# Performance work log

Hardware: AMD Instinct MI355X
Metric: run time of the kernel (lower is better)

Reference implementation:

```python
import jax, jax.numpy as jnp
import numpy as np

DIM = 1024
NUM_HEADS = 16
HEAD_DIM = DIM // NUM_HEADS

def setup_inputs() -> dict:
    key = jax.random.key(0)
    ks = jax.random.split(key, 5)
    s = 1.0 / np.sqrt(DIM)
    x = jax.random.normal(ks[0], (2, 2048, DIM), dtype=jnp.float32)
    W_qkv = jax.random.uniform(ks[1], (DIM, 3 * DIM), dtype=jnp.float32, minval=-s, maxval=s)
    b_qkv = jax.random.uniform(ks[2], (3 * DIM,), dtype=jnp.float32, minval=-s, maxval=s)
    W_out = jax.random.uniform(ks[3], (DIM, DIM), dtype=jnp.float32, minval=-s, maxval=s)
    b_out = jax.random.uniform(ks[4], (DIM,), dtype=jnp.float32, minval=-s, maxval=s)
    return {"x": x, "W_qkv": W_qkv, "b_qkv": b_qkv, "W_out": W_out, "b_out": b_out}

def reference(x, W_qkv, b_qkv, W_out, b_out):
    B, S, _ = x.shape
    qkv = x @ W_qkv + b_qkv                       # [B,S,3*dim]
    q, k, v = jnp.split(qkv, 3, axis=-1)
    # [B,S,dim] -> [B,H,S,hd]
    def to_heads(t):
        return t.reshape(B, S, NUM_HEADS, HEAD_DIM).transpose(0, 2, 1, 3)
    q, k, v = to_heads(q), to_heads(k), to_heads(v)
    scale = HEAD_DIM ** -0.5
    scores = jnp.einsum('bhqd,bhkd->bhqk', q, k) * scale
    attn = jax.nn.softmax(scores, axis=-1)
    out = jnp.einsum('bhqk,bhkd->bhqd', attn, v)  # [B,H,S,hd]
    out = out.transpose(0, 2, 1, 3).reshape(B, S, DIM)
    return out @ W_out + b_out
```

## Files before the change

kernel.cpp:

```cpp
#include <hip/hip_runtime.h>
#include <math.h>

#define DIMM    1024
#define NHEADS  16
#define HDIM    64
#define BATCH   2
#define SEQ     2048
#define ROWS    (BATCH*SEQ)

typedef _Float16 f16x8 __attribute__((ext_vector_type(8)));
typedef _Float16 f16x4 __attribute__((ext_vector_type(4)));
typedef _Float16 f16x2 __attribute__((ext_vector_type(2)));
typedef float    f32x4 __attribute__((ext_vector_type(4)));
typedef float    f32x16 __attribute__((ext_vector_type(16)));

__device__ inline void gl_lds16(const void* g, void* l) {
    __builtin_amdgcn_global_load_lds(
        (const __attribute__((address_space(1))) void*)g,
        (__attribute__((address_space(3))) void*)l, 16, 0, 0);
}

static __device__ inline f16x8 mkfrag(unsigned a, unsigned b, unsigned c, unsigned d) {
    union { unsigned u[4]; f16x8 v; } x;
    x.u[0] = a; x.u[1] = b; x.u[2] = c; x.u[3] = d;
    return x.v;
}

__device__ void tcvt64(const float* __restrict__ in, _Float16* __restrict__ out,
                       int K, int N, int k0, int n0, float (*tile)[65], int t)
{
    {
        const int c4 = (t & 15) * 4;
        const int r  = t >> 4;
        #pragma unroll
        for (int i = 0; i < 4; i++) {
            const int rr = r + 16 * i;
            float4 v = *(const float4*)(in + (size_t)(k0 + rr) * N + n0 + c4);
            tile[rr][c4] = v.x; tile[rr][c4 + 1] = v.y;
            tile[rr][c4 + 2] = v.z; tile[rr][c4 + 3] = v.w;
        }
    }
    __syncthreads();
    #pragma unroll
    for (int i = 0; i < 2; i++) {
        const int seg = t + 256 * i;
        const int n   = seg >> 3;
        const int kc  = (seg & 7) * 8;
        f16x8 o;
        #pragma unroll
        for (int j = 0; j < 8; j++) o[j] = (_Float16)tile[kc + j][n];
        *(f16x8*)(out + (size_t)(n0 + n) * K + k0 + kc) = o;
    }
}

__global__ __launch_bounds__(256)
void prep_kernel(const float* __restrict__ x, const float* __restrict__ Wqkv,
                 const float* __restrict__ Wout, _Float16* __restrict__ xh,
                 _Float16* __restrict__ wqkvt, _Float16* __restrict__ woutt)
{
    __shared__ float tile[64][65];
    const int bx = blockIdx.x;
    const int t  = threadIdx.x;
    if (bx < 2048) {
        const int i = bx * 256 + t;
        const float4 a = *(const float4*)(x + (size_t)i * 8);
        const float4 b = *(const float4*)(x + (size_t)i * 8 + 4);
        f16x8 o;
        o[0] = (_Float16)a.x; o[1] = (_Float16)a.y; o[2] = (_Float16)a.z; o[3] = (_Float16)a.w;
        o[4] = (_Float16)b.x; o[5] = (_Float16)b.y; o[6] = (_Float16)b.z; o[7] = (_Float16)b.w;
        *(f16x8*)(xh + (size_t)i * 8) = o;
    } else if (bx < 2816) {
        const int id = bx - 2048;
        const int gx = id % 48, gy = id / 48;
        tcvt64(Wqkv, wqkvt, DIMM, 3 * DIMM, gy * 64, gx * 64, tile, t);
    } else {
        const int id = bx - 2816;
        const int gx = id & 15, gy = id >> 4;
        tcvt64(Wout, woutt, DIMM, DIMM, gy * 64, gx * 64, tile, t);
    }
}

template<int OUT_F16, int BM, int FUSEVT>
__global__ __launch_bounds__(256)
void hgemm_db_kernel(const _Float16* __restrict__ A, const _Float16* __restrict__ Bt,
                     const float* __restrict__ bias, void* __restrict__ Cout,
                     _Float16* __restrict__ vtg, int N, int K)
{
    constexpr int MI = BM / 32;
    __shared__ _Float16 As[2][BM * 64];
    __shared__ _Float16 Bs[2][128 * 64];

    const int t    = threadIdx.x;
    const int w    = t >> 6, lane = t & 63;
    const int quad = lane >> 4, l16 = lane & 15;
    const int wr   = w >> 1, wc = w & 1;
    const int row0 = blockIdx.y * BM, col0 = blockIdx.x * 128;
    const int sw   = l16 & 7;

    f32x4 acc[MI][4];
    #pragma unroll
    for (int i = 0; i < MI; i++)
        #pragma unroll
        for (int j = 0; j < 4; j++)
            #pragma unroll
            for (int r = 0; r < 4; r++) acc[i][j][r] = 0.f;

    const _Float16* gA[MI];
    int aofs[MI];
    #pragma unroll
    for (int j = 0; j < MI; j++) {
        const int s   = t + 256 * j;
        const int row = s >> 3;
        const int kb  = (s & 7) ^ (row & 7);
        gA[j] = A + (size_t)(row0 + row) * K + kb * 8;
        aofs[j] = s * 8;
    }
    const _Float16* gB[4];
    int bofs[4];
    #pragma unroll
    for (int j = 0; j < 4; j++) {
        const int s   = t + 256 * j;
        const int row = s >> 3;
        const int kb  = (s & 7) ^ (row & 7);
        gB[j] = Bt + (size_t)(col0 + row) * K + kb * 8;
        bofs[j] = s * 8;
    }

    #pragma unroll
    for (int j = 0; j < MI; j++) gl_lds16(gA[j], &As[0][aofs[j]]);
    #pragma unroll
    for (int j = 0; j < 4; j++)  gl_lds16(gB[j], &Bs[0][bofs[j]]);
    #pragma unroll
    for (int j = 0; j < MI; j++) gA[j] += 64;
    #pragma unroll
    for (int j = 0; j < 4; j++)  gB[j] += 64;

    const int niter = K >> 6;
    #pragma unroll 1
    for (int it = 0; it < niter; it++) {
        const int cur = it & 1;
        __syncthreads();

        if (it + 1 < niter) {
            const int nxt = cur ^ 1;
            #pragma unroll
            for (int j = 0; j < MI; j++) gl_lds16(gA[j], &As[nxt][aofs[j]]);
            #pragma unroll
            for (int j = 0; j < 4; j++)  gl_lds16(gB[j], &Bs[nxt][bofs[j]]);
            #pragma unroll
            for (int j = 0; j < MI; j++) gA[j] += 64;
            #pragma unroll
            for (int j = 0; j < 4; j++)  gB[j] += 64;
        }

        const _Float16* AsC = &As[cur][0];
        const _Float16* BsC = &Bs[cur][0];
        f16x8 af[MI][2], bf[4][2];
        #pragma unroll
        for (int i = 0; i < MI; i++) {
            const int arow = wr * (BM / 2) + i * 16 + l16;
            #pragma unroll
            for (int hh = 0; hh < 2; hh++)
                af[i][hh] = *(const f16x8*)(AsC + (arow * 8 + ((hh * 4 + quad) ^ sw)) * 8);
        }
        #pragma unroll
        for (int j = 0; j < 4; j++) {
            const int brow = wc * 64 + j * 16 + l16;
            #pragma unroll
            for (int hh = 0; hh < 2; hh++)
                bf[j][hh] = *(const f16x8*)(BsC + (brow * 8 + ((hh * 4 + quad) ^ sw)) * 8);
        }
        #pragma unroll
        for (int i = 0; i < MI; i++)
            #pragma unroll
            for (int j = 0; j < 4; j++) {
                acc[i][j] = __builtin_amdgcn_mfma_f32_16x16x32_f16(af[i][0], bf[j][0], acc[i][j], 0, 0, 0);
                acc[i][j] = __builtin_amdgcn_mfma_f32_16x16x32_f16(af[i][1], bf[j][1], acc[i][j], 0, 0, 0);
            }
    }

    if (FUSEVT && blockIdx.x >= 16) {
        #pragma unroll
        for (int j = 0; j < 4; j++) {
            const int col = col0 + wc * 64 + j * 16 + l16;
            const float bv = bias[col];
            const int hv = (col - 2048) >> 6;
            const int dv = col & 63;
            #pragma unroll
            for (int i = 0; i < MI; i++) {
                const int row = row0 + wr * (BM / 2) + i * 16 + quad * 4;
                const int bb  = row >> 11;
                const int key = row & 2047;
                f16x4 o;
                #pragma unroll
                for (int r = 0; r < 4; r++) o[r] = (_Float16)(acc[i][j][r] + bv);
                *(f16x4*)(vtg + ((size_t)(bb * 16 + hv) * 64 + dv) * SEQ + key) = o;
            }
        }
        return;
    }

    #pragma unroll
    for (int j = 0; j < 4; j++) {
        const int col = col0 + wc * 64 + j * 16 + l16;
        const float bv = bias[col];
        #pragma unroll
        for (int i = 0; i < MI; i++) {
            const int row = row0 + wr * (BM / 2) + i * 16 + quad * 4;
            #pragma unroll
            for (int r = 0; r < 4; r++) {
                const float v = acc[i][j][r] + bv;
                if (OUT_F16)
                    ((_Float16*)Cout)[(size_t)(row + r) * N + col] = (_Float16)v;
                else
                    ((float*)Cout)[(size_t)(row + r) * N + col] = v;
            }
        }
    }
}

__global__ __launch_bounds__(256, 4)
void flash_attn_kernel(const _Float16* __restrict__ qkv,
                       const _Float16* __restrict__ vtg,
                       _Float16* __restrict__ out)
{
    const int qt = blockIdx.x;
    const int bh = blockIdx.y;
    const int b  = bh >> 4, hd = bh & 15;
    const int t    = threadIdx.x;
    const int w    = t >> 6;
    const int lane = t & 63;
    const int qg   = w >> 1;
    const int kh   = w & 1;
    const int l31  = lane & 31;
    const int hf   = lane >> 5;
    const int l7   = lane & 7;

    __shared__ __align__(16) _Float16 Ks [2][64 * 64];
    __shared__ __align__(16) _Float16 Vts[2][64 * 64];

    const int q0 = qt * 64;
    const size_t rstr = 3 * DIMM;
    const _Float16* qbase = qkv + (size_t)b * SEQ * rstr;

    f16x8 qf[4];
    {
        const _Float16* qrow = qbase + (size_t)(q0 + qg * 32 + l31) * rstr + hd * HDIM;
        #pragma unroll
        for (int dd = 0; dd < 4; dd++)
            qf[dd] = *(const f16x8*)(qrow + dd * 16 + hf * 8);
    }

    f32x16 Oacc[2];
    #pragma unroll
    for (int dh = 0; dh < 2; dh++)
        #pragma unroll
        for (int r = 0; r < 16; r++) Oacc[dh][r] = 0.f;
    float lrow = 0.f;

    const int seg0 = t, seg1 = t + 256;
    const int r0 = seg0 >> 3, lb0 = (seg0 & 7) ^ (r0 & 7);
    const int r1 = seg1 >> 3, lb1 = (seg1 & 7) ^ (r1 & 7);
    const _Float16* gK0 = qbase + (size_t)r0 * rstr + DIMM + hd * HDIM + lb0 * 8;
    const _Float16* gK1 = qbase + (size_t)r1 * rstr + DIMM + hd * HDIM + lb1 * 8;
    const _Float16* gV0 = vtg + ((size_t)bh * 64 + r0) * SEQ + lb0 * 8;
    const _Float16* gV1 = vtg + ((size_t)bh * 64 + r1) * SEQ + lb1 * 8;

    gl_lds16(gK0, &Ks [0][seg0 * 8]);
    gl_lds16(gK1, &Ks [0][seg1 * 8]);
    gl_lds16(gV0, &Vts[0][seg0 * 8]);
    gl_lds16(gV1, &Vts[0][seg1 * 8]);

    #pragma unroll 2
    for (int k0 = 0; k0 < SEQ; k0 += 64) {
        const int cur = (k0 >> 6) & 1;
        const _Float16* KsC  = &Ks [cur][0];
        const _Float16* VtsC = &Vts[cur][0];

        __syncthreads();

        f32x16 sacc;
        #pragma unroll
        for (int r = 0; r < 16; r++) sacc[r] = 0.f;
        #pragma unroll
        for (int dd = 0; dd < 4; dd++) {
            f16x8 kf = *(const f16x8*)(KsC + (kh * 32 + l31) * 64 + (((dd * 2 + hf) ^ l7) * 8));
            sacc = __builtin_amdgcn_mfma_f32_32x32x16_f16(kf, qf[dd], sacc, 0, 0, 0);
        }

        if (k0 + 64 < SEQ) {
            const int nxt = cur ^ 1;
            gl_lds16(gK0 + (size_t)(k0 + 64) * rstr, &Ks [nxt][seg0 * 8]);
            gl_lds16(gK1 + (size_t)(k0 + 64) * rstr, &Ks [nxt][seg1 * 8]);
            gl_lds16(gV0 + (k0 + 64),                &Vts[nxt][seg0 * 8]);
            gl_lds16(gV1 + (k0 + 64),                &Vts[nxt][seg1 * 8]);
        }

        float e[16];
        #pragma unroll
        for (int r = 0; r < 16; r++) {
            e[r] = __expf(sacc[r] * 0.125f);
            lrow += e[r];
        }

        unsigned w01 = __builtin_bit_cast(unsigned, __builtin_amdgcn_cvt_pkrtz(e[0],  e[1]));
        unsigned w23 = __builtin_bit_cast(unsigned, __builtin_amdgcn_cvt_pkrtz(e[2],  e[3]));
        unsigned w45 = __builtin_bit_cast(unsigned, __builtin_amdgcn_cvt_pkrtz(e[4],  e[5]));
        unsigned w67 = __builtin_bit_cast(unsigned, __builtin_amdgcn_cvt_pkrtz(e[6],  e[7]));
        unsigned w89 = __builtin_bit_cast(unsigned, __builtin_amdgcn_cvt_pkrtz(e[8],  e[9]));
        unsigned wab = __builtin_bit_cast(unsigned, __builtin_amdgcn_cvt_pkrtz(e[10], e[11]));
        unsigned wcd = __builtin_bit_cast(unsigned, __builtin_amdgcn_cvt_pkrtz(e[12], e[13]));
        unsigned wef = __builtin_bit_cast(unsigned, __builtin_amdgcn_cvt_pkrtz(e[14], e[15]));
        unsigned p00 = w01, p02 = w45;
        asm("v_permlane32_swap_b32 %0, %1" : "+v"(p00), "+v"(p02));
        unsigned p01 = w23, p03 = w67;
        asm("v_permlane32_swap_b32 %0, %1" : "+v"(p01), "+v"(p03));
        unsigned p10 = w89, p12 = wcd;
        asm("v_permlane32_swap_b32 %0, %1" : "+v"(p10), "+v"(p12));
        unsigned p11 = wab, p13 = wef;
        asm("v_permlane32_swap_b32 %0, %1" : "+v"(p11), "+v"(p13));
        f16x8 pa0 = mkfrag(p00, p01, p02, p03);
        f16x8 pa1 = mkfrag(p10, p11, p12, p13);

        #pragma unroll
        for (int dh = 0; dh < 2; dh++) {
            const _Float16* vrow = VtsC + (dh * 32 + l31) * 64;
            f16x8 vf0 = *(const f16x8*)(vrow + (((kh * 4 + 0 + hf) ^ l7) * 8));
            f16x8 vf1 = *(const f16x8*)(vrow + (((kh * 4 + 2 + hf) ^ l7) * 8));
            Oacc[dh] = __builtin_amdgcn_mfma_f32_32x32x16_f16(pa0, vf0, Oacc[dh], 0, 0, 0);
            Oacc[dh] = __builtin_amdgcn_mfma_f32_32x32x16_f16(pa1, vf1, Oacc[dh], 0, 0, 0);
        }
    }

    float lsum = lrow + __shfl_xor(lrow, 32);
    __syncthreads();
    float* Obuf = (float*)&Ks[0][0];
    float* lbuf = (float*)&Vts[0][0];
    if (kh) {
        #pragma unroll
        for (int dh = 0; dh < 2; dh++)
            #pragma unroll
            for (int r = 0; r < 16; r++) {
                const int q = (r & 3) + 8 * (r >> 2) + 4 * hf;
                Obuf[(qg * 32 + q) * 64 + dh * 32 + l31] = Oacc[dh][r];
            }
        if (lane < 32) lbuf[qg * 32 + lane] = lsum;
    }
    __syncthreads();
    if (!kh) {
        const float dnrec = 1.f / (lsum + lbuf[qg * 32 + l31]);
        float dq[16];
        #pragma unroll
        for (int r = 0; r < 16; r++)
            dq[r] = __shfl(dnrec, (r & 3) + 8 * (r >> 2) + 4 * hf);
        #pragma unroll
        for (int dh = 0; dh < 2; dh++)
            #pragma unroll
            for (int r = 0; r < 16; r++) {
                const int q = (r & 3) + 8 * (r >> 2) + 4 * hf;
                const float v = (Oacc[dh][r] + Obuf[(qg * 32 + q) * 64 + dh * 32 + l31])
                                * dq[r];
                out[(size_t)(b * SEQ + q0 + qg * 32 + q) * DIMM + hd * HDIM + dh * 32 + l31] =
                    (_Float16)v;
            }
    }
}

extern "C" void kernel_launch(void* const* d_in, const int* in_sizes, int n_in,
                              void* d_out, int out_size, void* d_ws, size_t ws_size,
                              hipStream_t stream)
{
    const float* x    = (const float*)d_in[0];
    const float* Wqkv = (const float*)d_in[1];
    const float* bqkv = (const float*)d_in[2];
    const float* Wout = (const float*)d_in[3];
    const float* bout = (const float*)d_in[4];
    float* out = (float*)d_out;

    _Float16* qkvh  = (_Float16*)d_ws;
    _Float16* attnh = qkvh  + (size_t)ROWS * 3 * DIMM;
    _Float16* xh    = attnh + (size_t)ROWS * DIMM;
    _Float16* wqkvt = xh    + (size_t)ROWS * DIMM;
    _Float16* woutt = wqkvt + (size_t)3 * DIMM * DIMM;
    _Float16* vtg   = woutt + (size_t)DIMM * DIMM;

    prep_kernel<<<3072, 256, 0, stream>>>(x, Wqkv, Wout, xh, wqkvt, woutt);
    {
        dim3 grid(3 * DIMM / 128, ROWS / 128);
        hgemm_db_kernel<1, 128, 1><<<grid, 256, 0, stream>>>(xh, wqkvt, bqkv, qkvh, vtg, 3 * DIMM, DIMM);
    }
    {
        dim3 grid(SEQ / 64, BATCH * NHEADS);
        flash_attn_kernel<<<grid, 256, 0, stream>>>(qkvh, vtg, attnh);
    }
    {
        dim3 grid(DIMM / 128, ROWS / 64);
        hgemm_db_kernel<0, 64, 0><<<grid, 256, 0, stream>>>(attnh, woutt, bout, out, nullptr, DIMM, DIMM);
    }
}
```

Baseline: 190.6 us.

## Use 256x256-tile 32x32 MFMA GEMM for QKV projection with LDS-staged V transpose

Replaces the QKV projection GEMM with a new kernel that uses 256x256 output tiles, 512 threads, 32x32x16 MFMA instructions and 128 KB of double-buffered LDS loaded through direct global-to-LDS copies. The larger tile raises arithmetic intensity and cuts redundant global loads. The V-transpose epilogue now stages results through swizzled LDS so it can write coalesced 16-byte rows into the transposed V buffer. The trade-off is much higher LDS use and far fewer blocks (12x16), which may leave CUs underoccupied. The output projection kernel is split out as a non-templated specialization.

```diff
diff --git a/kernel.cpp b/kernel.cpp
--- a/kernel.cpp
+++ b/kernel.cpp
@@ -10,7 +10,6 @@
 
 typedef _Float16 f16x8 __attribute__((ext_vector_type(8)));
 typedef _Float16 f16x4 __attribute__((ext_vector_type(4)));
-typedef _Float16 f16x2 __attribute__((ext_vector_type(2)));
 typedef float    f32x4 __attribute__((ext_vector_type(4)));
 typedef float    f32x16 __attribute__((ext_vector_type(16)));
 
@@ -80,13 +79,139 @@
     }
 }
 
-template<int OUT_F16, int BM, int FUSEVT>
+__global__ __launch_bounds__(512)
+void hgemm256_kernel(const _Float16* __restrict__ A, const _Float16* __restrict__ Bt,
+                     const float* __restrict__ bias, _Float16* __restrict__ C,
+                     _Float16* __restrict__ vtg, int N, int K)
+{
+    __shared__ __align__(16) _Float16 lds[65536];
+
+    const int t    = threadIdx.x;
+    const int w    = t >> 6, lane = t & 63;
+    const int l31  = lane & 31;
+    const int hf   = lane >> 5;
+    const int l7   = lane & 7;
+    const int wm   = w >> 2;
+    const int wn   = w & 3;
+    const int row0 = blockIdx.y * 256, col0 = blockIdx.x * 256;
+
+    f32x16 acc[4][2];
+    #pragma unroll
+    for (int mi = 0; mi < 4; mi++)
+        #pragma unroll
+        for (int ni = 0; ni < 2; ni++)
+            #pragma unroll
+            for (int r = 0; r < 16; r++) acc[mi][ni][r] = 0.f;
+
+    const _Float16* gA[4];
+    const _Float16* gB[4];
+    int sofs[4];
+    #pragma unroll
+    for (int j = 0; j < 4; j++) {
+        const int s   = t + 512 * j;
+        const int row = s >> 3;
+        const int kb  = (s & 7) ^ (row & 7);
+        gA[j] = A  + (size_t)(row0 + row) * K + kb * 8;
+        gB[j] = Bt + (size_t)(col0 + row) * K + kb * 8;
+        sofs[j] = s * 8;
+    }
+
+    #pragma unroll
+    for (int j = 0; j < 4; j++) gl_lds16(gA[j], lds + sofs[j]);
+    #pragma unroll
+    for (int j = 0; j < 4; j++) gl_lds16(gB[j], lds + 32768 + sofs[j]);
+    #pragma unroll
+    for (int j = 0; j < 4; j++) { gA[j] += 64; gB[j] += 64; }
+
+    const int niter = K >> 6;
+    #pragma unroll 1
+    for (int it = 0; it < niter; it++) {
+        const int cur = it & 1;
+        __syncthreads();
+
+        if (it + 1 < niter) {
+            const int nxt = cur ^ 1;
+            #pragma unroll
+            for (int j = 0; j < 4; j++) gl_lds16(gA[j], lds + nxt * 16384 + sofs[j]);
+            #pragma unroll
+            for (int j = 0; j < 4; j++) gl_lds16(gB[j], lds + 32768 + nxt * 16384 + sofs[j]);
+            #pragma unroll
+            for (int j = 0; j < 4; j++) { gA[j] += 64; gB[j] += 64; }
+        }
+
+        const _Float16* AsC = lds + cur * 16384;
+        const _Float16* BsC = lds + 32768 + cur * 16384;
+        #pragma unroll
+        for (int ks = 0; ks < 4; ks++) {
+            const int pseg = ((ks * 2 + hf) ^ l7) * 8;
+            f16x8 bf0 = *(const f16x8*)(BsC + (wn * 64 +      l31) * 64 + pseg);
+            f16x8 bf1 = *(const f16x8*)(BsC + (wn * 64 + 32 + l31) * 64 + pseg);
+            #pragma unroll
+            for (int mi = 0; mi < 4; mi++) {
+                f16x8 af = *(const f16x8*)(AsC + (wm * 128 + mi * 32 + l31) * 64 + pseg);
+                acc[mi][0] = __builtin_amdgcn_mfma_f32_32x32x16_f16(af, bf0, acc[mi][0], 0, 0, 0);
+                acc[mi][1] = __builtin_amdgcn_mfma_f32_32x32x16_f16(af, bf1, acc[mi][1], 0, 0, 0);
+            }
+        }
+    }
+
+    float bv[2];
+    #pragma unroll
+    for (int ni = 0; ni < 2; ni++) bv[ni] = bias[col0 + wn * 64 + ni * 32 + l31];
+
+    if (blockIdx.x < 8) {
+        #pragma unroll
+        for (int mi = 0; mi < 4; mi++)
+            #pragma unroll
+            for (int ni = 0; ni < 2; ni++) {
+                const int col = col0 + wn * 64 + ni * 32 + l31;
+                #pragma unroll
+                for (int r = 0; r < 16; r++) {
+                    const int row = row0 + wm * 128 + mi * 32 + (r & 3) + 8 * (r >> 2) + 4 * hf;
+                    C[(size_t)row * N + col] = (_Float16)(acc[mi][ni][r] + bv[ni]);
+                }
+            }
+        return;
+    }
+
+    __syncthreads();
+    #pragma unroll
+    for (int mi = 0; mi < 4; mi++)
+        #pragma unroll
+        for (int ni = 0; ni < 2; ni++) {
+            const int coll = wn * 64 + ni * 32 + l31;
+            #pragma unroll
+            for (int rq = 0; rq < 4; rq++) {
+                f16x4 o;
+                #pragma unroll
+                for (int ri = 0; ri < 4; ri++) o[ri] = (_Float16)(acc[mi][ni][rq * 4 + ri] + bv[ni]);
+                const int sidx = rq + 4 * mi + 16 * wm;
+                *(f16x4*)(lds + coll * 256 + ((sidx ^ (coll & 31)) << 3) + 4 * hf) = o;
+            }
+        }
+    __syncthreads();
+    {
+        const int cl   = t >> 1;
+        const int half = t & 1;
+        const int head = ((blockIdx.x - 8) << 2) + (cl >> 6);
+        const int dv   = cl & 63;
+        const int bb   = blockIdx.y >> 3;
+        const int key0 = (blockIdx.y & 7) * 256 + half * 128;
+        _Float16* dst = vtg + ((size_t)(bb * 16 + head) * 64 + dv) * SEQ + key0;
+        #pragma unroll
+        for (int c = 0; c < 16; c++) {
+            const int cs = half * 16 + c;
+            *(f16x8*)(dst + c * 8) = *(const f16x8*)(lds + cl * 256 + ((cs ^ (cl & 31)) << 3));
+        }
+    }
+}
+
 __global__ __launch_bounds__(256)
-void hgemm_db_kernel(const _Float16* __restrict__ A, const _Float16* __restrict__ Bt,
-                     const float* __restrict__ bias, void* __restrict__ Cout,
-                     _Float16* __restrict__ vtg, int N, int K)
-{
-    constexpr int MI = BM / 32;
+void hgemm_out_kernel(const _Float16* __restrict__ A, const _Float16* __restrict__ Bt,
+                      const float* __restrict__ bias, float* __restrict__ Cout,
+                      int N, int K)
+{
+    constexpr int BM = 64, MI = 2;
     __shared__ _Float16 As[2][BM * 64];
     __shared__ _Float16 Bs[2][128 * 64];
 
@@ -179,27 +304,6 @@
             }
     }
 
-    if (FUSEVT && blockIdx.x >= 16) {
-        #pragma unroll
-        for (int j = 0; j < 4; j++) {
-            const int col = col0 + wc * 64 + j * 16 + l16;
-            const float bv = bias[col];
-            const int hv = (col - 2048) >> 6;
-            const int dv = col & 63;
-            #pragma unroll
-            for (int i = 0; i < MI; i++) {
-                const int row = row0 + wr * (BM / 2) + i * 16 + quad * 4;
-                const int bb  = row >> 11;
-                const int key = row & 2047;
-                f16x4 o;
-                #pragma unroll
-                for (int r = 0; r < 4; r++) o[r] = (_Float16)(acc[i][j][r] + bv);
-                *(f16x4*)(vtg + ((size_t)(bb * 16 + hv) * 64 + dv) * SEQ + key) = o;
-            }
-        }
-        return;
-    }
-
     #pragma unroll
     for (int j = 0; j < 4; j++) {
         const int col = col0 + wc * 64 + j * 16 + l16;
@@ -208,13 +312,8 @@
         for (int i = 0; i < MI; i++) {
             const int row = row0 + wr * (BM / 2) + i * 16 + quad * 4;
             #pragma unroll
-            for (int r = 0; r < 4; r++) {
-                const float v = acc[i][j][r] + bv;
-                if (OUT_F16)
-                    ((_Float16*)Cout)[(size_t)(row + r) * N + col] = (_Float16)v;
-                else
-                    ((float*)Cout)[(size_t)(row + r) * N + col] = v;
-            }
+            for (int r = 0; r < 4; r++)
+                Cout[(size_t)(row + r) * N + col] = acc[i][j][r] + bv;
         }
     }
 }
@@ -386,8 +485,8 @@
 
     prep_kernel<<<3072, 256, 0, stream>>>(x, Wqkv, Wout, xh, wqkvt, woutt);
     {
-        dim3 grid(3 * DIMM / 128, ROWS / 128);
-        hgemm_db_kernel<1, 128, 1><<<grid, 256, 0, stream>>>(xh, wqkvt, bqkv, qkvh, vtg, 3 * DIMM, DIMM);
+        dim3 grid(3 * DIMM / 256, ROWS / 256);
+        hgemm256_kernel<<<grid, 512, 0, stream>>>(xh, wqkvt, bqkv, qkvh, vtg, 3 * DIMM, DIMM);
     }
     {
         dim3 grid(SEQ / 64, BATCH * NHEADS);
@@ -395,6 +494,6 @@
     }
     {
         dim3 grid(DIMM / 128, ROWS / 64);
-        hgemm_db_kernel<0, 64, 0><<<grid, 256, 0, stream>>>(attnh, woutt, bout, out, nullptr, DIMM, DIMM);
-    }
-}
+        hgemm_out_kernel<<<grid, 256, 0, stream>>>(attnh, woutt, bout, out, DIMM, DIMM);
+    }
+}
```

Result: no change. 187.3 us (-1.8%).
